# Kernel tuning notes

Measured on AMD Instinct MI355X. Metric: run time of the kernel, lower is better.

## Reference

```python
import jax, jax.numpy as jnp
import numpy as np

B, N, K = 32, 1024, 20          # graphs, points per graph, kNN neighbors
EMB = 1024                       # emb_dims
OUT = 7                          # out_channels
WS1, ST1, G1 = 52, 20, 7         # linear1 STFT-KAN: window, stride, gridsize
WS2, ST2, G2 = 197, 7, 6         # linear2 STFT-KAN
NW1 = (128 - WS1) // ST1 + 1     # 4 windows over 128-dim features
NW2 = (2 * EMB - WS2) // ST2 + 1 # 265 windows over 2048-dim features


def _window(kind, M):
    n = jnp.arange(M, dtype=jnp.float32)
    if kind == 'bartlett':
        return 1.0 - jnp.abs(2.0 * n / M - 1.0)        # periodic bartlett (torch default)
    return 0.5 * (1.0 - jnp.cos(2.0 * jnp.pi * n / M)) # periodic hann


def _stft_kan(x, coeffs, bias, gridsize, ws, stride, wtype):
    """x: [B, D]; coeffs: [2, outdim, nw, ws, gridsize]; returns [B, outdim]."""
    D = x.shape[1]
    nw = (D - ws) // stride + 1
    idx = jnp.arange(nw)[:, None] * stride + jnp.arange(ws)[None, :]  # [nw, ws]
    xw = x[:, idx] * _window(wtype, ws)                               # [B, nw, ws]
    kk = jnp.arange(1, gridsize + 1, dtype=x.dtype)
    ang = xw[..., None] * kk                                          # [B, nw, ws, g]
    y = jnp.einsum('bnwg,onwg->bo', jnp.cos(ang), coeffs[0])
    y = y + jnp.einsum('bnwg,onwg->bo', jnp.sin(ang), coeffs[1])
    return y + bias


def setup_inputs() -> dict:
    key = jax.random.key(0)
    ks = jax.random.split(key, 8)
    pos = jax.random.normal(ks[0], (B * N, 3), jnp.float32)
    batch = jnp.repeat(jnp.arange(B, dtype=jnp.int32), N)  # sorted, equal-size graphs
    # EdgeConv MLP([6,64,128]): Linear+BN+ReLU, then plain Linear
    W1 = jax.random.normal(ks[1], (6, 64), jnp.float32) * 0.3
    b1 = jnp.zeros((64,), jnp.float32)
    gamma1 = jnp.ones((64,), jnp.float32)
    beta1 = jnp.zeros((64,), jnp.float32)
    W2 = jax.random.normal(ks[2], (64, 128), jnp.float32) * 0.1
    b2 = jnp.zeros((128,), jnp.float32)
    # STFT-KAN 1 (smooth init: coeffs damped by k^2)
    k1 = np.arange(1, G1 + 1, dtype=np.float32)
    c1 = jax.random.normal(ks[3], (2, EMB, NW1, WS1, G1), jnp.float32) / (np.sqrt(NW1 * WS1) * (k1 ** 2))
    bi1 = jnp.zeros((EMB,), jnp.float32)
    # STFT-KAN 2 (non-smooth init)
    c2 = jax.random.normal(ks[4], (2, OUT, NW2, WS2, G2), jnp.float32) / (np.sqrt(NW2 * WS2) * np.sqrt(G2))
    bi2 = jnp.zeros((OUT,), jnp.float32)
    return {"pos": pos, "batch": batch, "W1": W1, "b1": b1, "gamma1": gamma1,
            "beta1": beta1, "W2": W2, "b2": b2, "c1": c1, "bi1": bi1, "c2": c2, "bi2": bi2}


def reference(pos, batch, W1, b1, gamma1, beta1, W2, b2, c1, bi1, c2, bi2):
    p = pos.reshape(B, N, 3)
    # dynamic kNN graph per batch element (exclude self)
    sq = jnp.sum(p * p, axis=-1)                                    # [B, N]
    d2 = sq[:, :, None] + sq[:, None, :] - 2.0 * jnp.einsum('bnd,bmd->bnm', p, p)
    d2 = d2 + jnp.eye(N, dtype=p.dtype) * 1e10
    _, idx = jax.lax.top_k(-d2, K)                                  # [B, N, K]
    pj = jax.vmap(lambda pts, ids: pts[ids])(p, idx)                # [B, N, K, 3]
    pi = jnp.broadcast_to(p[:, :, None, :], (B, N, K, 3))
    e = jnp.concatenate([pi, pj - pi], axis=-1)                     # [B, N, K, 6]
    # edge MLP: Linear -> BN -> ReLU -> Linear
    h = e @ W1 + b1
    mu = h.mean((0, 1, 2))
    var = h.var((0, 1, 2))
    h = gamma1 * (h - mu) * jax.lax.rsqrt(var + 1e-5) + beta1
    h = jax.nn.relu(h)
    h = h @ W2 + b2                                                 # [B, N, K, 128]
    x1 = h.max(axis=2).reshape(B * N, 128)                          # max aggregation over neighbors
    x = _stft_kan(x1, c1, bi1, G1, WS1, ST1, 'bartlett')            # [B*N, EMB]
    xg = x.reshape(B, N, EMB)
    xcat = jnp.concatenate([xg.max(axis=1), xg.mean(axis=1)], axis=-1)  # global max/mean pool
    return _stft_kan(xcat, c2, bi2, G2, WS2, ST2, 'hann')           # [B, OUT]
```

## Files before the change

### kernel.cpp

```cpp
#include <hip/hip_runtime.h>
#include <cstdint>

typedef _Float16 half8 __attribute__((ext_vector_type(8)));
typedef __fp16 fp16x2 __attribute__((ext_vector_type(2)));
typedef float f32x2 __attribute__((ext_vector_type(2)));
typedef float f32x4 __attribute__((ext_vector_type(4)));

__device__ __forceinline__ void gload16(const void* g, void* l) {
  __builtin_amdgcn_global_load_lds(
      (const __attribute__((address_space(1))) void*)g,
      (__attribute__((address_space(3))) void*)l, 16, 0, 0);
}

template <int CTRL, int RM>
__device__ __forceinline__ void dppmin(float& d, int& j) {
  int di = __builtin_amdgcn_update_dpp(__float_as_int(d), __float_as_int(d), CTRL, RM, 0xf, false);
  int ji = __builtin_amdgcn_update_dpp(j, j, CTRL, RM, 0xf, false);
  float df = __int_as_float(di);
  bool c = (df < d) || (df == d && ji < j);
  d = c ? df : d;
  j = c ? ji : j;
}

__global__ __launch_bounds__(256) void knn_kernel(const float* __restrict__ pos,
                                                  int* __restrict__ nbr) {
  __shared__ float4 pts[1024];
  int tid = threadIdx.x;
  int b = blockIdx.x >> 8;
  const float* pg = pos + (size_t)b * 3072;
  for (int m = 0; m < 4; ++m) {
    int j = m * 256 + tid;
    float x = pg[3 * j], y = pg[3 * j + 1], z = pg[3 * j + 2];
    pts[j] = make_float4(x, y, z, x * x + y * y + z * z);
  }
  __syncthreads();
  int wave = tid >> 6, lane = tid & 63;
  int n = (blockIdx.x & 255) * 4 + wave;
  float4 pn = pts[n];
  float d[16];
#pragma unroll
  for (int i = 0; i < 16; ++i) {
    int j = i * 64 + lane;
    float4 pj = pts[j];
    float dd = pn.w + pj.w - 2.0f * (pn.x * pj.x + pn.y * pj.y + pn.z * pj.z);
    d[i] = (j == n) ? 1e30f : dd;
  }
  int outbase = (b * 1024 + n) * 20;
  for (int kk = 0; kk < 20; ++kk) {
    float v8[8]; int i8[8];
#pragma unroll
    for (int i = 0; i < 8; ++i) {
      bool c = d[2 * i + 1] < d[2 * i];
      v8[i] = c ? d[2 * i + 1] : d[2 * i];
      i8[i] = c ? (2 * i + 1) : (2 * i);
    }
    float v4[4]; int i4[4];
#pragma unroll
    for (int i = 0; i < 4; ++i) {
      bool c = v8[2 * i + 1] < v8[2 * i];
      v4[i] = c ? v8[2 * i + 1] : v8[2 * i];
      i4[i] = c ? i8[2 * i + 1] : i8[2 * i];
    }
    float v2[2]; int i2[2];
#pragma unroll
    for (int i = 0; i < 2; ++i) {
      bool c = v4[2 * i + 1] < v4[2 * i];
      v2[i] = c ? v4[2 * i + 1] : v4[2 * i];
      i2[i] = c ? i4[2 * i + 1] : i4[2 * i];
    }
    bool ctop = v2[1] < v2[0];
    float bv = ctop ? v2[1] : v2[0];
    int bi = (ctop ? i2[1] : i2[0]) * 64 + lane;
    dppmin<0xB1, 0xf>(bv, bi);
    dppmin<0x4E, 0xf>(bv, bi);
    dppmin<0x141, 0xf>(bv, bi);
    dppmin<0x140, 0xf>(bv, bi);
    dppmin<0x142, 0xa>(bv, bi);
    dppmin<0x143, 0xc>(bv, bi);
    int widx = __builtin_amdgcn_readlane(bi, 63);
    if (lane == 0) nbr[outbase + kk] = b * 1024 + widx;
    if ((widx & 63) == lane) {
      int rp = widx >> 6;
#pragma unroll
      for (int i = 0; i < 16; ++i)
        if (i == rp) d[i] = 1e30f;
    }
  }
}

__global__ __launch_bounds__(256) void edge_stats_kernel(
    const float* __restrict__ pos, const int* __restrict__ nbr,
    const float* __restrict__ W1, const float* __restrict__ b1v,
    float* __restrict__ psum, float* __restrict__ psq) {
  __shared__ float els[256][6];
  __shared__ float w1s[384];
  __shared__ float b1s[64];
  __shared__ float red[8][64];
  int tid = threadIdx.x, bid = blockIdx.x;
  for (int f = tid; f < 384; f += 256) w1s[f] = W1[f];
  if (tid < 64) b1s[tid] = b1v[tid];
  int c = tid & 63, grp = tid >> 6;
  float s = 0.f, s2 = 0.f;
  for (int ch = 0; ch < 5; ++ch) {
    int E = bid * 1280 + ch * 256 + tid;
    int p = E / 20;
    int j = nbr[E];
    float pix = pos[3 * p], piy = pos[3 * p + 1], piz = pos[3 * p + 2];
    float e3 = pos[3 * j] - pix, e4 = pos[3 * j + 1] - piy, e5 = pos[3 * j + 2] - piz;
    __syncthreads();
    els[tid][0] = pix; els[tid][1] = piy; els[tid][2] = piz;
    els[tid][3] = e3;  els[tid][4] = e4;  els[tid][5] = e5;
    __syncthreads();
    for (int m = 0; m < 64; ++m) {
      int e = grp * 64 + m;
      float h = b1s[c];
#pragma unroll
      for (int dd = 0; dd < 6; ++dd) h += els[e][dd] * w1s[dd * 64 + c];
      s += h; s2 += h * h;
    }
  }
  red[grp][c] = s;
  __syncthreads();
  red[4 + grp][c] = s2;
  __syncthreads();
  if (tid < 64) {
    float S = red[0][tid] + red[1][tid] + red[2][tid] + red[3][tid];
    float Q = red[4][tid] + red[5][tid] + red[6][tid] + red[7][tid];
    psum[bid * 64 + tid] = S;
    psq[bid * 64 + tid] = Q;
  }
}

__global__ void bn_finalize_kernel(const float* __restrict__ psum, const float* __restrict__ psq,
                                   const float* __restrict__ gamma, const float* __restrict__ beta,
                                   float* __restrict__ bns, float* __restrict__ bnh) {
  int c = threadIdx.x;
  float s = 0.f, q = 0.f;
  for (int b = 0; b < 512; ++b) { s += psum[b * 64 + c]; q += psq[b * 64 + c]; }
  const float inv = 1.0f / 655360.0f;
  float mu = s * inv;
  float var = q * inv - mu * mu;
  float sc = gamma[c] * rsqrtf(var + 1e-5f);
  bns[c] = sc;
  bnh[c] = beta[c] - mu * sc;
}

__global__ __launch_bounds__(256) void edge_mlp_kernel(
    const float* __restrict__ pos, const int* __restrict__ nbr,
    const float* __restrict__ W1, const float* __restrict__ b1v,
    const float* __restrict__ bns, const float* __restrict__ bnh,
    const float* __restrict__ W2, const float* __restrict__ b2v,
    float* __restrict__ x1) {
  __shared__ __align__(16) char elds[53248];
  _Float16* Ah = (_Float16*)(elds);
  _Float16* Al = (_Float16*)(elds + 10240);
  _Float16* Bh = (_Float16*)(elds + 20480);
  _Float16* Bl = (_Float16*)(elds + 36864);
  float* outb = (float*)elds;
  __shared__ float w1s[384];
  __shared__ float b1s[64], scs[64], shs[64];
  int tid = threadIdx.x, bid = blockIdx.x;
  for (int f = tid; f < 384; f += 256) w1s[f] = W1[f];
  if (tid < 64) { b1s[tid] = b1v[tid]; scs[tid] = bns[tid]; shs[tid] = bnh[tid]; }
#pragma unroll
  for (int i = 0; i < 32; ++i) {
    int flat = tid + 256 * i;
    int dd = flat >> 7, c = flat & 127;
    float v = W2[flat];
    _Float16 hi = (_Float16)v;
    _Float16 lo = (_Float16)(v - (float)hi);
    int byte = c * 128 + ((((dd >> 3) ^ (c & 7))) << 4) + (dd & 7) * 2;
    *(_Float16*)((char*)Bh + byte) = hi;
    *(_Float16*)((char*)Bl + byte) = lo;
  }
  __syncthreads();
#pragma unroll
  for (int m = 0; m < 20; ++m) {
    int flat = tid + 256 * m;
    int row = flat >> 6;
    int d = flat & 63;
    int j = nbr[bid * 80 + row];
    int P = bid * 4 + (row / 20);
    float pix = pos[3 * P], piy = pos[3 * P + 1], piz = pos[3 * P + 2];
    float e3 = pos[3 * j] - pix, e4 = pos[3 * j + 1] - piy, e5 = pos[3 * j + 2] - piz;
    float h = b1s[d];
    h += pix * w1s[d] + piy * w1s[64 + d] + piz * w1s[128 + d]
       + e3 * w1s[192 + d] + e4 * w1s[256 + d] + e5 * w1s[320 + d];
    h = scs[d] * h + shs[d];
    h = fmaxf(h, 0.f);
    _Float16 hi = (_Float16)h;
    _Float16 lo = (_Float16)(h - (float)hi);
    int byte = row * 128 + ((((d >> 3) ^ (row & 7))) << 4) + (d & 7) * 2;
    *(_Float16*)((char*)Ah + byte) = hi;
    *(_Float16*)((char*)Al + byte) = lo;
  }
  __syncthreads();
  int wave = tid >> 6, lane = tid & 63;
  int l15 = lane & 15, l4 = lane >> 4;
  f32x4 acc[5][2] = {};
#pragma unroll
  for (int ks = 0; ks < 2; ++ks) {
    int slotk = ks * 4 + l4;
    half8 bfh[2], bfl[2];
#pragma unroll
    for (int ci = 0; ci < 2; ++ci) {
      int col = (wave * 2 + ci) * 16 + l15;
      int byte = col * 128 + ((slotk ^ (col & 7)) << 4);
      bfh[ci] = *(const half8*)((char*)Bh + byte);
      bfl[ci] = *(const half8*)((char*)Bl + byte);
    }
#pragma unroll
    for (int rt = 0; rt < 5; ++rt) {
      int row = rt * 16 + l15;
      int byte = row * 128 + ((slotk ^ (row & 7)) << 4);
      half8 ah = *(const half8*)((char*)Ah + byte);
      half8 al = *(const half8*)((char*)Al + byte);
#pragma unroll
      for (int ci = 0; ci < 2; ++ci) {
        acc[rt][ci] = __builtin_amdgcn_mfma_f32_16x16x32_f16(ah, bfh[ci], acc[rt][ci], 0, 0, 0);
        acc[rt][ci] = __builtin_amdgcn_mfma_f32_16x16x32_f16(ah, bfl[ci], acc[rt][ci], 0, 0, 0);
        acc[rt][ci] = __builtin_amdgcn_mfma_f32_16x16x32_f16(al, bfh[ci], acc[rt][ci], 0, 0, 0);
      }
    }
  }
  __syncthreads();
#pragma unroll
  for (int rt = 0; rt < 5; ++rt)
#pragma unroll
    for (int ci = 0; ci < 2; ++ci) {
      int col = (wave * 2 + ci) * 16 + l15;
#pragma unroll
      for (int q = 0; q < 4; ++q) {
        int row = rt * 16 + l4 * 4 + q;
        outb[row * 129 + col] = acc[rt][ci][q];
      }
    }
  __syncthreads();
#pragma unroll
  for (int r = 0; r < 2; ++r) {
    int it = tid + 256 * r;
    int p = it >> 7, c = it & 127;
    float mx = -1e30f;
#pragma unroll
    for (int e = 0; e < 20; ++e) mx = fmaxf(mx, outb[(p * 20 + e) * 129 + c]);
    x1[((size_t)bid * 4 + p) * 128 + c] = mx + b2v[c];
  }
}

__global__ void c1_to_f16_kernel(const float* __restrict__ c1, _Float16* __restrict__ Cf) {
  int L = blockIdx.x * 256 + threadIdx.x;
  if (L >= 1024 * 3328) return;
  int o = L / 3328, rem = L % 3328;
  int t = rem >> 6, idx = rem & 63;
  int s = idx >> 3, e = idx & 7;
  int half = s >> 2, n = s & 3;
  float v = 0.0f;
  if (!(half == 1 && e >= 6)) {
    int phase = e & 1;
    int g0 = half * 4 + (e >> 1);
    v = c1[((((size_t)phase * 1024 + o) * 4 + n) * 52 + t) * 7 + g0];
  }
  Cf[L] = (_Float16)v;
}

#define AGEN_PAIR(XV, BART, O0, O1) do {                                 \
    float th_ = (XV) * (BART);                                           \
    float sn_, cs_;                                                      \
    __sincosf(th_, &sn_, &cs_);                                          \
    float c2s_ = cs_ + cs_;                                              \
    f32x2 c2v_ = {c2s_, c2s_};                                           \
    f32x2 p1_ = {cs_, sn_};                                              \
    f32x2 p2_ = c2v_ * p1_ - (f32x2){1.0f, 0.0f};                        \
    f32x2 p3_ = c2v_ * p2_ - p1_;                                        \
    f32x2 p4_ = c2v_ * p3_ - p2_;                                        \
    f32x2 p5_ = c2v_ * p4_ - p3_;                                        \
    f32x2 p6_ = c2v_ * p5_ - p4_;                                        \
    f32x2 p7_ = c2v_ * p6_ - p5_;                                        \
    union { half8 v; fp16x2 q[4]; } u0_, u1_;                            \
    u0_.q[0] = __builtin_amdgcn_cvt_pkrtz(p1_.x, p1_.y);                 \
    u0_.q[1] = __builtin_amdgcn_cvt_pkrtz(p2_.x, p2_.y);                 \
    u0_.q[2] = __builtin_amdgcn_cvt_pkrtz(p3_.x, p3_.y);                 \
    u0_.q[3] = __builtin_amdgcn_cvt_pkrtz(p4_.x, p4_.y);                 \
    u1_.q[0] = __builtin_amdgcn_cvt_pkrtz(p5_.x, p5_.y);                 \
    u1_.q[1] = __builtin_amdgcn_cvt_pkrtz(p6_.x, p6_.y);                 \
    u1_.q[2] = __builtin_amdgcn_cvt_pkrtz(p7_.x, p7_.y);                 \
    u1_.q[3] = (fp16x2){(__fp16)0.0f, (__fp16)0.0f};                     \
    (O0) = u0_.v;                                                        \
    (O1) = u1_.v;                                                        \
  } while (0)

#define MFMA_PHASE_SGB(BUF, A0, A1) do {                                          \
    half8 bf_[4];                                                                 \
    _Pragma("unroll")                                                             \
    for (int ni = 0; ni < 4; ++ni) {                                              \
      int col = wc * 64 + ni * 16 + l15;                                          \
      bf_[ni] = *(const half8*)((char*)Bsm[BUF] + col * 128 + ((l4 ^ (col & 7)) << 4)); \
    }                                                                             \
    _Pragma("unroll")                                                             \
    for (int mi = 0; mi < 4; ++mi)                                                \
      _Pragma("unroll")                                                           \
      for (int ni = 0; ni < 4; ++ni)                                              \
        acc[mi][ni] = __builtin_amdgcn_mfma_f32_16x16x32_f16(A0[mi], bf_[ni], acc[mi][ni], 0, 0, 0); \
    _Pragma("unroll")                                                             \
    for (int ni = 0; ni < 4; ++ni) {                                              \
      int col = wc * 64 + ni * 16 + l15;                                          \
      bf_[ni] = *(const half8*)((char*)Bsm[BUF] + col * 128 + (((4 + l4) ^ (col & 7)) << 4)); \
    }                                                                             \
    _Pragma("unroll")                                                             \
    for (int mi = 0; mi < 4; ++mi)                                                \
      _Pragma("unroll")                                                           \
      for (int ni = 0; ni < 4; ++ni)                                              \
        acc[mi][ni] = __builtin_amdgcn_mfma_f32_16x16x32_f16(A1[mi], bf_[ni], acc[mi][ni], 0, 0, 0); \
    __builtin_amdgcn_sched_group_barrier(0x100, 4, 0);                            \
    _Pragma("unroll")                                                             \
    for (int r_ = 0; r_ < 16; ++r_) {                                             \
      __builtin_amdgcn_sched_group_barrier(0x008, 1, 0);                          \
      __builtin_amdgcn_sched_group_barrier(0x002, 4, 0);                          \
    }                                                                             \
    __builtin_amdgcn_sched_group_barrier(0x100, 4, 0);                            \
    _Pragma("unroll")                                                             \
    for (int r_ = 0; r_ < 16; ++r_) {                                             \
      __builtin_amdgcn_sched_group_barrier(0x008, 1, 0);                          \
      __builtin_amdgcn_sched_group_barrier(0x002, 4, 0);                          \
    }                                                                             \
  } while (0)

__global__ __launch_bounds__(512, 2) void kan1_gemm_kernel(
    const float* __restrict__ x1, const _Float16* __restrict__ Cf,
    float* __restrict__ pmax, float* __restrict__ psump) {
  __shared__ __align__(16) _Float16 Bsm[2][128 * 64];
  int tid = threadIdx.x;
  int bm = blockIdx.x, bn = blockIdx.y;
  int m0 = bm << 8, n0 = bn << 7;
  int wave = tid >> 6, lane = tid & 63;
  int wr = wave >> 1, wc = wave & 1;
  int l15 = lane & 15, l4 = lane >> 4;

  auto stageB = [&](int t, int nb) {
    int j0 = t << 6;
#pragma unroll
    for (int i = 0; i < 2; ++i) {
      int idx = i * 512 + tid;
      int col = idx >> 3, slot = idx & 7;
      int sslot = slot ^ (col & 7);
      gload16(Cf + (size_t)(n0 + col) * 3328 + j0 + sslot * 8,
              (char*)Bsm[nb] + idx * 16);
    }
  };

  const float* xbase = x1 + (size_t)(m0 + wr * 64 + l15) * 128 + l4 * 20;
  half8 aC0[4], aC1[4], aN0[4], aN1[4];
  float xC[4], xN[4];
  f32x4 acc[4][4] = {};

#pragma unroll
  for (int mi = 0; mi < 4; ++mi) xC[mi] = xbase[mi * 2048];
  stageB(0, 0);
  {
    const float bart0 = 0.0f;
#pragma unroll
    for (int mi = 0; mi < 4; ++mi) AGEN_PAIR(xC[mi], bart0, aC0[mi], aC1[mi]);
  }
#pragma unroll
  for (int mi = 0; mi < 4; ++mi) { xN[mi] = xbase[mi * 2048 + 1]; xC[mi] = xbase[mi * 2048 + 2]; }
  __syncthreads();

  for (int i = 0; i < 26; ++i) {
    {
      stageB(2 * i + 1, 1);
      float bart = 1.0f - fabsf((float)(2 * (2 * i + 1)) * (1.0f / 52.0f) - 1.0f);
#pragma unroll
      for (int mi = 0; mi < 4; ++mi) AGEN_PAIR(xN[mi], bart, aN0[mi], aN1[mi]);
      int nx = 2 * i + 3; nx = nx > 51 ? 51 : nx;
#pragma unroll
      for (int mi = 0; mi < 4; ++mi) xN[mi] = xbase[mi * 2048 + nx];
      MFMA_PHASE_SGB(0, aC0, aC1);
      __syncthreads();
    }
    {
      int ts = 2 * i + 2; ts = ts > 51 ? 51 : ts;
      stageB(ts, 0);
      float bart = 1.0f - fabsf((float)(2 * ts) * (1.0f / 52.0f) - 1.0f);
#pragma unroll
      for (int mi = 0; mi < 4; ++mi) AGEN_PAIR(xC[mi], bart, aC0[mi], aC1[mi]);
      int nx = 2 * i + 4; nx = nx > 51 ? 51 : nx;
#pragma unroll
      for (int mi = 0; mi < 4; ++mi) xC[mi] = xbase[mi * 2048 + nx];
      MFMA_PHASE_SGB(1, aN0, aN1);
      __syncthreads();
    }
  }

  float* pooled = (float*)Bsm;
#pragma unroll
  for (int ni = 0; ni < 4; ++ni) {
    float mx = -1e30f, sm = 0.f;
#pragma unroll
    for (int mi = 0; mi < 4; ++mi)
#pragma unroll
      for (int q = 0; q < 4; ++q) {
        float v = acc[mi][ni][q];
        mx = fmaxf(mx, v); sm += v;
      }
    mx = fmaxf(mx, __shfl_xor(mx, 16)); sm += __shfl_xor(sm, 16);
    mx = fmaxf(mx, __shfl_xor(mx, 32)); sm += __shfl_xor(sm, 32);
    if (l4 == 0) {
      int col = wc * 64 + ni * 16 + l15;
      pooled[(wr * 2 + 0) * 128 + col] = mx;
      pooled[(wr * 2 + 1) * 128 + col] = sm;
    }
  }
  __syncthreads();
  if (tid < 128) {
    float mx = pooled[tid], sm = pooled[128 + tid];
#pragma unroll
    for (int w = 1; w < 4; ++w) {
      mx = fmaxf(mx, pooled[(w * 2 + 0) * 128 + tid]);
      sm += pooled[(w * 2 + 1) * 128 + tid];
    }
    pmax[(size_t)bm * 1024 + n0 + tid] = mx;
    psump[(size_t)bm * 1024 + n0 + tid] = sm;
  }
}

__global__ void pool_reduce_kernel(const float* __restrict__ pmax, const float* __restrict__ psump,
                                   const float* __restrict__ bi1,
                                   float* __restrict__ gmax, float* __restrict__ gmean) {
  int gid = blockIdx.x * 256 + threadIdx.x;
  int b = gid >> 10, col = gid & 1023;
  float mx = -1e30f, sm = 0.f;
  for (int t = 0; t < 4; ++t) {
    mx = fmaxf(mx, pmax[(size_t)(b * 4 + t) * 1024 + col]);
    sm += psump[(size_t)(b * 4 + t) * 1024 + col];
  }
  float bias = bi1[col];
  gmax[gid] = mx + bias;
  gmean[gid] = sm * (1.0f / 1024.0f) + bias;
}

__global__ __launch_bounds__(256) void kan2_kernel(
    const float* __restrict__ gmax, const float* __restrict__ gmean,
    const float* __restrict__ c2, float* __restrict__ part) {
  __shared__ float xc[2048];
  __shared__ float hw[197];
  __shared__ float racc[7][256];
  int b = blockIdx.x, s = blockIdx.y, tid = threadIdx.x;
  for (int f = tid; f < 1024; f += 256) {
    xc[f] = gmax[b * 1024 + f];
    xc[1024 + f] = gmean[b * 1024 + f];
  }
  for (int f = tid; f < 197; f += 256)
    hw[f] = 0.5f * (1.0f - cosf(6.283185307179586f * (float)f / 197.0f));
  float acc[7] = {};
  __syncthreads();
  int qlo = (52205 * s) / 16, qhi = (52205 * (s + 1)) / 16;
  for (int q = qlo + tid; q < qhi; q += 256) {
    int n = q / 197;
    int w = q - n * 197;
    float xw = xc[n * 7 + w] * hw[w];
    float s1, c1v;
    __sincosf(xw, &s1, &c1v);
    float ckv[6], skv[6];
    {
      float ck = c1v, sk = s1;
#pragma unroll
      for (int g = 0; g < 6; ++g) {
        ckv[g] = ck; skv[g] = sk;
        float cn = ck * c1v - sk * s1;
        sk = sk * c1v + ck * s1;
        ck = cn;
      }
    }
    int base = q * 6;
#pragma unroll
    for (int o = 0; o < 7; ++o) {
      const float* pc = c2 + (size_t)o * 313230 + base;
      const float* ps = c2 + (size_t)(o + 7) * 313230 + base;
      float sc = 0.f, ss = 0.f;
#pragma unroll
      for (int g = 0; g < 6; ++g) { sc += ckv[g] * pc[g]; ss += skv[g] * ps[g]; }
      acc[o] += sc + ss;
    }
  }
#pragma unroll
  for (int o = 0; o < 7; ++o) racc[o][tid] = acc[o];
  __syncthreads();
  for (int st = 128; st >= 1; st >>= 1) {
    if (tid < st)
#pragma unroll
      for (int o = 0; o < 7; ++o) racc[o][tid] += racc[o][tid + st];
    __syncthreads();
  }
  if (tid < 7) part[(b * 16 + s) * 7 + tid] = racc[tid][0];
}

__global__ void kan2_reduce_kernel(const float* __restrict__ part, const float* __restrict__ bi2,
                                   float* __restrict__ out) {
  int i = threadIdx.x;
  if (i >= 224) return;
  int b = i / 7, o = i % 7;
  float s = 0.f;
  for (int t = 0; t < 16; ++t) s += part[(b * 16 + t) * 7 + o];
  out[b * 7 + o] = s + bi2[o];
}

extern "C" void kernel_launch(void* const* d_in, const int* in_sizes, int n_in,
                              void* d_out, int out_size, void* d_ws, size_t ws_size,
                              hipStream_t stream) {
  const float* pos    = (const float*)d_in[0];
  const float* W1     = (const float*)d_in[2];
  const float* b1     = (const float*)d_in[3];
  const float* gamma1 = (const float*)d_in[4];
  const float* beta1  = (const float*)d_in[5];
  const float* W2     = (const float*)d_in[6];
  const float* b2     = (const float*)d_in[7];
  const float* c1     = (const float*)d_in[8];
  const float* bi1    = (const float*)d_in[9];
  const float* c2     = (const float*)d_in[10];
  const float* bi2    = (const float*)d_in[11];
  float* out = (float*)d_out;
  char* ws = (char*)d_ws;

  int*      nbr   = (int*)     (ws + 0);
  float*    x1    = (float*)   (ws + 2621440);
  _Float16* Cf    = (_Float16*)(ws + 19398656);
  float*    psum  = (float*)   (ws + 26214400);
  float*    psq   = (float*)   (ws + 26345472);
  float*    bns   = (float*)   (ws + 26476544);
  float*    bnh   = (float*)   (ws + 26476800);
  float*    pmax  = (float*)   (ws + 26477056);
  float*    psump = (float*)   (ws + 27001344);
  float*    gmax  = (float*)   (ws + 27525632);
  float*    gmean = (float*)   (ws + 27656704);
  float*    part  = (float*)   (ws + 27787776);
  if (ws_size < 27802112) return;

  knn_kernel<<<8192, 256, 0, stream>>>(pos, nbr);
  c1_to_f16_kernel<<<13312, 256, 0, stream>>>(c1, Cf);
  edge_stats_kernel<<<512, 256, 0, stream>>>(pos, nbr, W1, b1, psum, psq);
  bn_finalize_kernel<<<1, 64, 0, stream>>>(psum, psq, gamma1, beta1, bns, bnh);
  edge_mlp_kernel<<<8192, 256, 0, stream>>>(pos, nbr, W1, b1, bns, bnh, W2, b2, x1);
  kan1_gemm_kernel<<<dim3(128, 8), 512, 0, stream>>>(x1, Cf, pmax, psump);
  pool_reduce_kernel<<<128, 256, 0, stream>>>(pmax, psump, bi1, gmax, gmean);
  kan2_kernel<<<dim3(32, 16), 256, 0, stream>>>(gmax, gmean, c2, part);
  kan2_reduce_kernel<<<1, 256, 0, stream>>>(part, bi2, out);
}
```

Before: 648.2 us.

## Load KAN1 B fragments directly from global in MFMA layout, drop LDS staging

Reorders the fp16 coefficient tensor so each tap's B fragments are contiguous per lane in MFMA operand order, letting the KAN1 GEMM read them straight from global/L2 into registers instead of staging through double-buffered LDS with barriers. The block shrinks to 256 threads with a 128-row tile (2048 blocks, occupancy hint 3), and the per-tile pooled partials double, so the pool reducer now sums 8 partials per graph. This removes LDS traffic and per-tap syncs but exposes global-load latency inside the MFMA loop without software prefetch, and each B fragment is re-read by more blocks.

Result: slower. 692.3 us (+6.8%).

```diff
diff --git a/kernel.cpp b/kernel.cpp
--- a/kernel.cpp
+++ b/kernel.cpp
@@ -5,12 +5,6 @@
 typedef __fp16 fp16x2 __attribute__((ext_vector_type(2)));
 typedef float f32x2 __attribute__((ext_vector_type(2)));
 typedef float f32x4 __attribute__((ext_vector_type(4)));
-
-__device__ __forceinline__ void gload16(const void* g, void* l) {
-  __builtin_amdgcn_global_load_lds(
-      (const __attribute__((address_space(1))) void*)g,
-      (__attribute__((address_space(3))) void*)l, 16, 0, 0);
-}
 
 template <int CTRL, int RM>
 __device__ __forceinline__ void dppmin(float& d, int& j) {
@@ -249,16 +243,17 @@
 
 __global__ void c1_to_f16_kernel(const float* __restrict__ c1, _Float16* __restrict__ Cf) {
   int L = blockIdx.x * 256 + threadIdx.x;
-  if (L >= 1024 * 3328) return;
-  int o = L / 3328, rem = L % 3328;
-  int t = rem >> 6, idx = rem & 63;
-  int s = idx >> 3, e = idx & 7;
+  int tap = L >> 16;
+  int r = L & 65535;
+  int s = r >> 13;
+  int o = (r >> 3) & 1023;
+  int e = r & 7;
   int half = s >> 2, n = s & 3;
   float v = 0.0f;
   if (!(half == 1 && e >= 6)) {
     int phase = e & 1;
     int g0 = half * 4 + (e >> 1);
-    v = c1[((((size_t)phase * 1024 + o) * 4 + n) * 52 + t) * 7 + g0];
+    v = c1[((((size_t)phase * 1024 + o) * 4 + n) * 52 + tap) * 7 + g0];
   }
   Cf[L] = (_Float16)v;
 }
@@ -289,109 +284,52 @@
     (O1) = u1_.v;                                                        \
   } while (0)
 
-#define MFMA_PHASE_SGB(BUF, A0, A1) do {                                          \
-    half8 bf_[4];                                                                 \
-    _Pragma("unroll")                                                             \
-    for (int ni = 0; ni < 4; ++ni) {                                              \
-      int col = wc * 64 + ni * 16 + l15;                                          \
-      bf_[ni] = *(const half8*)((char*)Bsm[BUF] + col * 128 + ((l4 ^ (col & 7)) << 4)); \
-    }                                                                             \
-    _Pragma("unroll")                                                             \
-    for (int mi = 0; mi < 4; ++mi)                                                \
-      _Pragma("unroll")                                                           \
-      for (int ni = 0; ni < 4; ++ni)                                              \
-        acc[mi][ni] = __builtin_amdgcn_mfma_f32_16x16x32_f16(A0[mi], bf_[ni], acc[mi][ni], 0, 0, 0); \
-    _Pragma("unroll")                                                             \
-    for (int ni = 0; ni < 4; ++ni) {                                              \
-      int col = wc * 64 + ni * 16 + l15;                                          \
-      bf_[ni] = *(const half8*)((char*)Bsm[BUF] + col * 128 + (((4 + l4) ^ (col & 7)) << 4)); \
-    }                                                                             \
-    _Pragma("unroll")                                                             \
-    for (int mi = 0; mi < 4; ++mi)                                                \
-      _Pragma("unroll")                                                           \
-      for (int ni = 0; ni < 4; ++ni)                                              \
-        acc[mi][ni] = __builtin_amdgcn_mfma_f32_16x16x32_f16(A1[mi], bf_[ni], acc[mi][ni], 0, 0, 0); \
-    __builtin_amdgcn_sched_group_barrier(0x100, 4, 0);                            \
-    _Pragma("unroll")                                                             \
-    for (int r_ = 0; r_ < 16; ++r_) {                                             \
-      __builtin_amdgcn_sched_group_barrier(0x008, 1, 0);                          \
-      __builtin_amdgcn_sched_group_barrier(0x002, 4, 0);                          \
-    }                                                                             \
-    __builtin_amdgcn_sched_group_barrier(0x100, 4, 0);                            \
-    _Pragma("unroll")                                                             \
-    for (int r_ = 0; r_ < 16; ++r_) {                                             \
-      __builtin_amdgcn_sched_group_barrier(0x008, 1, 0);                          \
-      __builtin_amdgcn_sched_group_barrier(0x002, 4, 0);                          \
-    }                                                                             \
-  } while (0)
-
-__global__ __launch_bounds__(512, 2) void kan1_gemm_kernel(
+__global__ __launch_bounds__(256, 3) void kan1_gemm_kernel(
     const float* __restrict__ x1, const _Float16* __restrict__ Cf,
     float* __restrict__ pmax, float* __restrict__ psump) {
-  __shared__ __align__(16) _Float16 Bsm[2][128 * 64];
+  __shared__ float pooled[512];
   int tid = threadIdx.x;
   int bm = blockIdx.x, bn = blockIdx.y;
-  int m0 = bm << 8, n0 = bn << 7;
+  int m0 = bm << 7, n0 = bn << 7;
   int wave = tid >> 6, lane = tid & 63;
   int wr = wave >> 1, wc = wave & 1;
   int l15 = lane & 15, l4 = lane >> 4;
 
-  auto stageB = [&](int t, int nb) {
-    int j0 = t << 6;
-#pragma unroll
-    for (int i = 0; i < 2; ++i) {
-      int idx = i * 512 + tid;
-      int col = idx >> 3, slot = idx & 7;
-      int sslot = slot ^ (col & 7);
-      gload16(Cf + (size_t)(n0 + col) * 3328 + j0 + sslot * 8,
-              (char*)Bsm[nb] + idx * 16);
-    }
-  };
-
   const float* xbase = x1 + (size_t)(m0 + wr * 64 + l15) * 128 + l4 * 20;
-  half8 aC0[4], aC1[4], aN0[4], aN1[4];
-  float xC[4], xN[4];
+  const _Float16* cfb = Cf + ((size_t)l4 * 1024 + n0 + wc * 64 + l15) * 8;
+
   f32x4 acc[4][4] = {};
-
+  float xC[4];
 #pragma unroll
   for (int mi = 0; mi < 4; ++mi) xC[mi] = xbase[mi * 2048];
-  stageB(0, 0);
-  {
-    const float bart0 = 0.0f;
-#pragma unroll
-    for (int mi = 0; mi < 4; ++mi) AGEN_PAIR(xC[mi], bart0, aC0[mi], aC1[mi]);
-  }
-#pragma unroll
-  for (int mi = 0; mi < 4; ++mi) { xN[mi] = xbase[mi * 2048 + 1]; xC[mi] = xbase[mi * 2048 + 2]; }
-  __syncthreads();
-
-  for (int i = 0; i < 26; ++i) {
-    {
-      stageB(2 * i + 1, 1);
-      float bart = 1.0f - fabsf((float)(2 * (2 * i + 1)) * (1.0f / 52.0f) - 1.0f);
-#pragma unroll
-      for (int mi = 0; mi < 4; ++mi) AGEN_PAIR(xN[mi], bart, aN0[mi], aN1[mi]);
-      int nx = 2 * i + 3; nx = nx > 51 ? 51 : nx;
-#pragma unroll
-      for (int mi = 0; mi < 4; ++mi) xN[mi] = xbase[mi * 2048 + nx];
-      MFMA_PHASE_SGB(0, aC0, aC1);
-      __syncthreads();
-    }
-    {
-      int ts = 2 * i + 2; ts = ts > 51 ? 51 : ts;
-      stageB(ts, 0);
-      float bart = 1.0f - fabsf((float)(2 * ts) * (1.0f / 52.0f) - 1.0f);
-#pragma unroll
-      for (int mi = 0; mi < 4; ++mi) AGEN_PAIR(xC[mi], bart, aC0[mi], aC1[mi]);
-      int nx = 2 * i + 4; nx = nx > 51 ? 51 : nx;
-#pragma unroll
-      for (int mi = 0; mi < 4; ++mi) xC[mi] = xbase[mi * 2048 + nx];
-      MFMA_PHASE_SGB(1, aN0, aN1);
-      __syncthreads();
-    }
-  }
-
-  float* pooled = (float*)Bsm;
+
+  for (int tap = 0; tap < 52; ++tap) {
+    float bart = 1.0f - fabsf((float)(2 * tap) * (1.0f / 52.0f) - 1.0f);
+    half8 a0[4], a1[4];
+#pragma unroll
+    for (int mi = 0; mi < 4; ++mi) AGEN_PAIR(xC[mi], bart, a0[mi], a1[mi]);
+    int nx = tap + 1; nx = nx > 51 ? 51 : nx;
+#pragma unroll
+    for (int mi = 0; mi < 4; ++mi) xC[mi] = xbase[mi * 2048 + nx];
+    const _Float16* bt = cfb + (size_t)tap * 65536;
+    half8 bf0[4], bf1[4];
+#pragma unroll
+    for (int ni = 0; ni < 4; ++ni) {
+      bf0[ni] = *(const half8*)(bt + ni * 128);
+      bf1[ni] = *(const half8*)(bt + 32768 + ni * 128);
+    }
+#pragma unroll
+    for (int mi = 0; mi < 4; ++mi)
+#pragma unroll
+      for (int ni = 0; ni < 4; ++ni)
+        acc[mi][ni] = __builtin_amdgcn_mfma_f32_16x16x32_f16(a0[mi], bf0[ni], acc[mi][ni], 0, 0, 0);
+#pragma unroll
+    for (int mi = 0; mi < 4; ++mi)
+#pragma unroll
+      for (int ni = 0; ni < 4; ++ni)
+        acc[mi][ni] = __builtin_amdgcn_mfma_f32_16x16x32_f16(a1[mi], bf1[ni], acc[mi][ni], 0, 0, 0);
+  }
+
 #pragma unroll
   for (int ni = 0; ni < 4; ++ni) {
     float mx = -1e30f, sm = 0.f;
@@ -412,12 +350,8 @@
   }
   __syncthreads();
   if (tid < 128) {
-    float mx = pooled[tid], sm = pooled[128 + tid];
-#pragma unroll
-    for (int w = 1; w < 4; ++w) {
-      mx = fmaxf(mx, pooled[(w * 2 + 0) * 128 + tid]);
-      sm += pooled[(w * 2 + 1) * 128 + tid];
-    }
+    float mx = fmaxf(pooled[tid], pooled[256 + tid]);
+    float sm = pooled[128 + tid] + pooled[384 + tid];
     pmax[(size_t)bm * 1024 + n0 + tid] = mx;
     psump[(size_t)bm * 1024 + n0 + tid] = sm;
   }
@@ -429,9 +363,9 @@
   int gid = blockIdx.x * 256 + threadIdx.x;
   int b = gid >> 10, col = gid & 1023;
   float mx = -1e30f, sm = 0.f;
-  for (int t = 0; t < 4; ++t) {
-    mx = fmaxf(mx, pmax[(size_t)(b * 4 + t) * 1024 + col]);
-    sm += psump[(size_t)(b * 4 + t) * 1024 + col];
+  for (int t = 0; t < 8; ++t) {
+    mx = fmaxf(mx, pmax[(size_t)(b * 8 + t) * 1024 + col]);
+    sm += psump[(size_t)(b * 8 + t) * 1024 + col];
   }
   float bias = bi1[col];
   gmax[gid] = mx + bias;
@@ -529,18 +463,18 @@
   float*    bns   = (float*)   (ws + 26476544);
   float*    bnh   = (float*)   (ws + 26476800);
   float*    pmax  = (float*)   (ws + 26477056);
-  float*    psump = (float*)   (ws + 27001344);
-  float*    gmax  = (float*)   (ws + 27525632);
-  float*    gmean = (float*)   (ws + 27656704);
-  float*    part  = (float*)   (ws + 27787776);
-  if (ws_size < 27802112) return;
+  float*    psump = (float*)   (ws + 27525632);
+  float*    gmax  = (float*)   (ws + 28574208);
+  float*    gmean = (float*)   (ws + 28705280);
+  float*    part  = (float*)   (ws + 28836352);
+  if (ws_size < 28850688) return;
 
   knn_kernel<<<8192, 256, 0, stream>>>(pos, nbr);
   c1_to_f16_kernel<<<13312, 256, 0, stream>>>(c1, Cf);
   edge_stats_kernel<<<512, 256, 0, stream>>>(pos, nbr, W1, b1, psum, psq);
   bn_finalize_kernel<<<1, 64, 0, stream>>>(psum, psq, gamma1, beta1, bns, bnh);
   edge_mlp_kernel<<<8192, 256, 0, stream>>>(pos, nbr, W1, b1, bns, bnh, W2, b2, x1);
-  kan1_gemm_kernel<<<dim3(128, 8), 512, 0, stream>>>(x1, Cf, pmax, psump);
+  kan1_gemm_kernel<<<dim3(256, 8), 256, 0, stream>>>(x1, Cf, pmax, psump);
   pool_reduce_kernel<<<128, 256, 0, stream>>>(pmax, psump, bi1, gmax, gmean);
   kan2_kernel<<<dim3(32, 16), 256, 0, stream>>>(gmax, gmean, c2, part);
   kan2_reduce_kernel<<<1, 256, 0, stream>>>(part, bi2, out);
```
